# Optimization experiments

Hardware: AMD Instinct MI355X
Metric: run time of the kernel (lower is better)

Reference implementation:

```python
import jax, jax.numpy as jnp
import numpy as np

HEADS = 8
DIM_HEAD = 64
QLEVEL = 127.0  # symmetric int8: clamp to [-128, 127]


def fake_quant(x):
    """Symmetric per-tensor int8 fake quantization with straight-through estimator."""
    delta = jnp.max(jnp.abs(x)) / QLEVEL
    xq = jnp.clip(jnp.round(x / delta), -128.0, 127.0) * delta
    return x + jax.lax.stop_gradient(xq - x)


def setup_inputs() -> dict:
    key = jax.random.key(0)
    ks = jax.random.split(key, 7)
    b, n, m, d, dc = 2, 4096, 1024, 512, 768
    return {
        "x": jax.random.normal(ks[0], (b, n, d), jnp.float32),
        "context": jax.random.normal(ks[1], (b, m, dc), jnp.float32),
        "Wq": jax.random.normal(ks[2], (d, d), jnp.float32) * 0.02,
        "Wk": jax.random.normal(ks[3], (dc, d), jnp.float32) * 0.02,
        "Wv": jax.random.normal(ks[4], (dc, d), jnp.float32) * 0.02,
        "Wo": jax.random.normal(ks[5], (d, d), jnp.float32) * 0.02,
        "bo": jnp.zeros((d,), jnp.float32),
    }


def reference(x, context, Wq, Wk, Wv, Wo, bo):
    b, n, _ = x.shape
    h, dh = HEADS, DIM_HEAD
    scale = dh ** -0.5

    q = x @ Wq            # [b, n, h*dh]
    k = context @ Wk      # [b, m, h*dh]
    v = context @ Wv      # [b, m, h*dh]

    def split(t):  # b n (h d) -> b h n d
        return t.reshape(t.shape[0], t.shape[1], h, dh).transpose(0, 2, 1, 3)

    q, k, v = split(q), split(k), split(v)

    # fake-quantize q and k before the score matmul (use_aq=True path)
    q = fake_quant(q)
    k = fake_quant(k)
    sim = jnp.einsum('bhid,bhjd->bhij', q, k) * scale  # [b, h, n, m]
    attn = jax.nn.softmax(sim, axis=-1)

    # fake-quantize attention weights and v before the AV matmul
    out = jnp.einsum('bhij,bhjd->bhid', fake_quant(attn), fake_quant(v))
    out = out.transpose(0, 2, 1, 3).reshape(b, n, h * dh)  # b h n d -> b n (h d)
    return out @ Wo + bo  # to_out[0]; to_out[-1] is Dropout (identity in eval)
```

## Files before the change

### kernel.cpp

```cpp
#include <hip/hip_runtime.h>
#include <stdint.h>

typedef float  v4f  __attribute__((ext_vector_type(4)));
typedef int    v4i  __attribute__((ext_vector_type(4)));
typedef __bf16 v8bf __attribute__((ext_vector_type(8)));
typedef __bf16 v4bf __attribute__((ext_vector_type(4)));

#define BATCH  2
#define NQ     4096
#define MK     1024
#define DMODEL 512
#define DCTX   768
#define NH     8
#define DH     64

__global__ __launch_bounds__(256) void k_wtrans(
    const float* __restrict__ Wq, const float* __restrict__ Wk,
    const float* __restrict__ Wv, const float* __restrict__ Wo,
    __bf16* __restrict__ Wq_t, __bf16* __restrict__ Wk_t,
    __bf16* __restrict__ Wv_t, __bf16* __restrict__ Wo_t,
    unsigned* __restrict__ scal) {
  if (blockIdx.x == 0 && blockIdx.y == 0 && blockIdx.z == 0 && threadIdx.x < 4)
    scal[threadIdx.x] = 0u;
  const float* src; __bf16* dst; int K;
  switch (blockIdx.z) {
    case 0:  src = Wq; dst = Wq_t; K = DMODEL; break;
    case 1:  src = Wk; dst = Wk_t; K = DCTX;   break;
    case 2:  src = Wv; dst = Wv_t; K = DCTX;   break;
    default: src = Wo; dst = Wo_t; K = DMODEL; break;
  }
  int k0 = blockIdx.y * 32;
  if (k0 >= K) return;
  int n0 = blockIdx.x * 32;
  __shared__ __bf16 tile[32][33];
  int c = threadIdx.x & 31, r0 = threadIdx.x >> 5;
  for (int i = 0; i < 4; ++i) {
    int r = r0 + i * 8;
    tile[c][r] = (__bf16)src[(size_t)(k0 + r) * DMODEL + n0 + c];
  }
  __syncthreads();
  for (int i = 0; i < 4; ++i) {
    int r = r0 + i * 8;
    dst[(size_t)(n0 + r) * K + k0 + c] = tile[r][c];
  }
}

__global__ __launch_bounds__(256) void k_cvt(
    const float* __restrict__ x, const float* __restrict__ ctx,
    __bf16* __restrict__ xb, __bf16* __restrict__ cb) {
  const int XC = BATCH * NQ * DMODEL / 8;
  const int CC = BATCH * MK * DCTX / 8;
  int idx = blockIdx.x * 256 + threadIdx.x;
  const float* src; __bf16* dst;
  if (idx < XC) { src = x + (size_t)idx * 8; dst = xb + (size_t)idx * 8; }
  else {
    int j = idx - XC;
    if (j >= CC) return;
    src = ctx + (size_t)j * 8; dst = cb + (size_t)j * 8;
  }
  float4 a = *(const float4*)src, b = *(const float4*)(src + 4);
  v8bf o = { (__bf16)a.x, (__bf16)a.y, (__bf16)a.z, (__bf16)a.w,
             (__bf16)b.x, (__bf16)b.y, (__bf16)b.z, (__bf16)b.w };
  *(v8bf*)dst = o;
}

template<int K_, bool BIAS, bool AMAX>
__global__ __launch_bounds__(256, 3) void k_gemm_bs(
    const __bf16* __restrict__ A, const __bf16* __restrict__ Bt,
    float* __restrict__ C, int M, int N,
    const float* __restrict__ bias,
    unsigned* __restrict__ amaxLo, unsigned* __restrict__ amaxHi) {
  constexpr int CS = K_ + 8;
  constexpr int GPC = K_ / 8;
  __shared__ __bf16 Bs[32 * CS];
  __shared__ float redmax[4];
  const int tid = threadIdx.x;
  const int lane = tid & 63, wave = tid >> 6;
  const int l15 = lane & 15, g = lane >> 4;
  const int col0 = blockIdx.y * 32;
  const int row0w = blockIdx.x * 128 + wave * 32;

#pragma unroll
  for (int i = 0; i < GPC * 32 / 256; ++i) {
    int f = i * 256 + tid;
    int c = f / GPC, w = f - c * GPC;
    *(v8bf*)(&Bs[c * CS + w * 8]) =
        *(const v8bf*)(Bt + (size_t)(col0 + c) * K_ + w * 8);
  }
  __syncthreads();

  v4f acc[2][2] = {};
  const __bf16* a0 = A + (size_t)(row0w + l15) * K_ + g * 8;
  const __bf16* a1 = A + (size_t)(row0w + 16 + l15) * K_ + g * 8;
#pragma unroll
  for (int k0 = 0; k0 < K_; k0 += 32) {
    v8bf af0 = *(const v8bf*)(a0 + k0);
    v8bf af1 = *(const v8bf*)(a1 + k0);
    v8bf bf0 = *(const v8bf*)(&Bs[l15 * CS + k0 + g * 8]);
    v8bf bf1 = *(const v8bf*)(&Bs[(16 + l15) * CS + k0 + g * 8]);
    acc[0][0] = __builtin_amdgcn_mfma_f32_16x16x32_bf16(af0, bf0, acc[0][0], 0, 0, 0);
    acc[0][1] = __builtin_amdgcn_mfma_f32_16x16x32_bf16(af0, bf1, acc[0][1], 0, 0, 0);
    acc[1][0] = __builtin_amdgcn_mfma_f32_16x16x32_bf16(af1, bf0, acc[1][0], 0, 0, 0);
    acc[1][1] = __builtin_amdgcn_mfma_f32_16x16x32_bf16(af1, bf1, acc[1][1], 0, 0, 0);
  }

  float lmax = 0.0f;
#pragma unroll
  for (int j = 0; j < 2; ++j) {
    int col = col0 + j * 16 + l15;
    float bv = BIAS ? bias[col] : 0.0f;
#pragma unroll
    for (int i = 0; i < 2; ++i) {
#pragma unroll
      for (int r = 0; r < 4; ++r) {
        int row = row0w + i * 16 + g * 4 + r;
        float cv = acc[i][j][r] + bv;
        C[(size_t)row * N + col] = cv;
        if (AMAX) lmax = fmaxf(lmax, fabsf(cv));
      }
    }
  }
  if (AMAX) {
    for (int off = 32; off > 0; off >>= 1)
      lmax = fmaxf(lmax, __shfl_xor(lmax, off, 64));
    if (lane == 0) redmax[wave] = lmax;
    __syncthreads();
    if (tid == 0) {
      float bm = fmaxf(fmaxf(redmax[0], redmax[1]), fmaxf(redmax[2], redmax[3]));
      atomicMax(col0 < 512 ? amaxLo : amaxHi, __float_as_uint(bm));
    }
  }
}

__global__ __launch_bounds__(256) void k_quant_kv(
    const float* __restrict__ kvf,
    int8_t* __restrict__ k8, int8_t* __restrict__ v8t,
    const unsigned* __restrict__ scal) {
  __shared__ int8_t tile[64][80];
  int bx = blockIdx.x;
  if (bx < 1024) {
    int j = bx * 256 + threadIdx.x;
    int r = j >> 7;
    int c4 = (j & 127) << 2;
    float4 v = *(const float4*)(kvf + (size_t)r * 1024 + c4);
    float s = 127.0f / __uint_as_float(scal[1]);
    int a0 = __float2int_rn(v.x * s), a1 = __float2int_rn(v.y * s);
    int a2 = __float2int_rn(v.z * s), a3 = __float2int_rn(v.w * s);
    a0 = max(-128, min(127, a0)); a1 = max(-128, min(127, a1));
    a2 = max(-128, min(127, a2)); a3 = max(-128, min(127, a3));
    unsigned p = (unsigned)(a0 & 255) | ((unsigned)(a1 & 255) << 8) |
                 ((unsigned)(a2 & 255) << 16) | ((unsigned)(a3 & 255) << 24);
    *(unsigned*)(k8 + (size_t)j * 4) = p;
    return;
  }
  int id = bx - 1024;
  int bh = id >> 4, b = bh >> 3, h = bh & 7;
  int j0 = (id & 15) * 64;
  const float s = 127.0f / __uint_as_float(scal[2]);
  int t = threadIdx.x;
  int j = t >> 2, dh0 = (t & 3) << 4;
  const float* src = kvf + (size_t)(b * MK + j0 + j) * 1024 + 512 + h * DH + dh0;
#pragma unroll
  for (int i = 0; i < 16; i += 4) {
    float4 v = *(const float4*)(src + i);
    int a0 = __float2int_rn(v.x * s), a1 = __float2int_rn(v.y * s);
    int a2 = __float2int_rn(v.z * s), a3 = __float2int_rn(v.w * s);
    tile[dh0 + i + 0][j] = (int8_t)max(-128, min(127, a0));
    tile[dh0 + i + 1][j] = (int8_t)max(-128, min(127, a1));
    tile[dh0 + i + 2][j] = (int8_t)max(-128, min(127, a2));
    tile[dh0 + i + 3][j] = (int8_t)max(-128, min(127, a3));
  }
  __syncthreads();
  int dh = t >> 2, jb = (t & 3) << 4;
  v4i val = *(const v4i*)(&tile[dh][jb]);
  *(v4i*)(v8t + (size_t)(bh * DH + dh) * MK + j0 + jb) = val;
}

__device__ __forceinline__ v4i quant_pack16(const float* p, float s) {
  v4i out;
#pragma unroll
  for (int q = 0; q < 4; ++q) {
    float4 v = *(const float4*)(p + q * 4);
    int a0 = __float2int_rn(v.x * s), a1 = __float2int_rn(v.y * s);
    int a2 = __float2int_rn(v.z * s), a3 = __float2int_rn(v.w * s);
    a0 = max(-128, min(127, a0)); a1 = max(-128, min(127, a1));
    a2 = max(-128, min(127, a2)); a3 = max(-128, min(127, a3));
    out[q] = (int)((unsigned)(a0 & 255) | ((unsigned)(a1 & 255) << 8) |
                   ((unsigned)(a2 & 255) << 16) | ((unsigned)(a3 & 255) << 24));
  }
  return out;
}

__global__ __launch_bounds__(256, 4) void k_pass1(
    const float* __restrict__ qf, int8_t* __restrict__ q8,
    const int8_t* __restrict__ k8,
    float* __restrict__ invz, unsigned* __restrict__ scal) {
  __shared__ float zbuf[4][64];
  __shared__ int   mbuf[4][64];
  int bh = blockIdx.y, b = bh >> 3, h = bh & 7;
  int wave = threadIdx.x >> 6, lane = threadIdx.x & 63;
  int l15 = lane & 15, g = lane >> 4;
  int row0 = blockIdx.x * 64;
  const float aq = __uint_as_float(scal[0]), ak = __uint_as_float(scal[1]);
  const float alpha2 = (aq * ak) * (0.125f / (127.0f * 127.0f)) * 1.44269504f;
  const float sq = 127.0f / aq;
  const v4i z4 = {0, 0, 0, 0};
  v4i qfrag[4];
#pragma unroll
  for (int rg = 0; rg < 4; ++rg) {
    size_t off = (size_t)(b * NQ + row0 + rg * 16 + l15) * DMODEL + h * DH + g * 16;
    qfrag[rg] = quant_pack16(qf + off, sq);
    *(v4i*)(q8 + off) = qfrag[rg];
  }
  const int8_t* kbase = k8 + (size_t)b * MK * DMODEL + h * DH + g * 16 +
                        (size_t)wave * 256 * DMODEL;
  v4i kf[16];
#pragma unroll
  for (int i = 0; i < 16; ++i)
    kf[i] = *(const v4i*)(kbase + (size_t)(i * 16 + l15) * DMODEL);

  float z[4] = {0.f, 0.f, 0.f, 0.f};
  int mi[4] = {-(1 << 30), -(1 << 30), -(1 << 30), -(1 << 30)};
#pragma unroll
  for (int kt = 0; kt < 16; ++kt) {
#pragma unroll
    for (int rg = 0; rg < 4; ++rg) {
      v4i sa = __builtin_amdgcn_mfma_i32_16x16x64_i8(kf[kt], qfrag[rg], z4, 0, 0, 0);
      mi[rg] = max(mi[rg], max(max(sa[0], sa[1]), max(sa[2], sa[3])));
      float e0 = __builtin_amdgcn_exp2f((float)sa[0] * alpha2);
      float e1 = __builtin_amdgcn_exp2f((float)sa[1] * alpha2);
      float e2 = __builtin_amdgcn_exp2f((float)sa[2] * alpha2);
      float e3 = __builtin_amdgcn_exp2f((float)sa[3] * alpha2);
      z[rg] += (e0 + e1) + (e2 + e3);
    }
  }
#pragma unroll
  for (int rg = 0; rg < 4; ++rg) {
    z[rg] += __shfl_xor(z[rg], 16, 64);
    mi[rg] = max(mi[rg], __shfl_xor(mi[rg], 16, 64));
    z[rg] += __shfl_xor(z[rg], 32, 64);
    mi[rg] = max(mi[rg], __shfl_xor(mi[rg], 32, 64));
  }
  if (lane < 16) {
#pragma unroll
    for (int rg = 0; rg < 4; ++rg) {
      zbuf[wave][rg * 16 + l15] = z[rg];
      mbuf[wave][rg * 16 + l15] = mi[rg];
    }
  }
  __syncthreads();
  if (threadIdx.x < 64) {
    int r = threadIdx.x;
    float zt = (zbuf[0][r] + zbuf[1][r]) + (zbuf[2][r] + zbuf[3][r]);
    int mt = max(max(mbuf[0][r], mbuf[1][r]), max(mbuf[2][r], mbuf[3][r]));
    float iz = 1.0f / zt;
    invz[(size_t)bh * NQ + row0 + r] = iz;
    float ma = __builtin_amdgcn_exp2f((float)mt * alpha2) * iz;
    for (int off = 1; off < 64; off <<= 1)
      ma = fmaxf(ma, __shfl_xor(ma, off, 64));
    if (r == 0) atomicMax(scal + 3, __float_as_uint(ma));
  }
}

__global__ __launch_bounds__(256, 2) void k_pass2(
    const int8_t* __restrict__ q8, const int8_t* __restrict__ k8,
    const int8_t* __restrict__ v8t, const float* __restrict__ invz,
    const unsigned* __restrict__ scal, __bf16* __restrict__ o) {
  __shared__ __align__(16) int8_t attn_lds[4][16 * 80];
  __shared__ __align__(16) int redbuf[16][64][4];
  int bh = blockIdx.y, b = bh >> 3, h = bh & 7;
  int wave = threadIdx.x >> 6, lane = threadIdx.x & 63;
  int l15 = lane & 15, g = lane >> 4;
  int row0 = blockIdx.x * 64;
  int key0 = wave * 256;
  const float aq = __uint_as_float(scal[0]), ak = __uint_as_float(scal[1]);
  const float avv = __uint_as_float(scal[2]), izm = __uint_as_float(scal[3]);
  const float alpha2 = (aq * ak) * (0.125f / (127.0f * 127.0f)) * 1.44269504f;
  const float oscale = (izm / 127.0f) * (avv / 127.0f);
  const float MAGIC = 12582912.0f;
  const v4i z4 = {0, 0, 0, 0};

  v4i qfrag[4];
  float lc[4];
#pragma unroll
  for (int rg = 0; rg < 4; ++rg) {
    qfrag[rg] = *(const v4i*)(q8 + (size_t)(b * NQ + row0 + rg * 16 + l15) * DMODEL + h * DH + g * 16);
    lc[rg] = __builtin_amdgcn_logf(invz[(size_t)bh * NQ + row0 + rg * 16 + l15] * (127.0f / izm));
  }
  const int8_t* kbase = k8 + (size_t)(b * MK + key0) * DMODEL + h * DH + g * 16;
  v4i kf[16];
#pragma unroll
  for (int i = 0; i < 16; ++i)
    kf[i] = *(const v4i*)(kbase + (size_t)(i * 16 + l15) * DMODEL);
  const int8_t* vbase = v8t + (size_t)bh * DH * MK + key0 + g * 16;
  v4i vf[16];
#pragma unroll
  for (int d = 0; d < 4; ++d)
#pragma unroll
    for (int c = 0; c < 4; ++c)
      vf[d * 4 + c] = *(const v4i*)(vbase + (size_t)(d * 16 + l15) * MK + c * 64);

  int8_t* alds = attn_lds[wave];
  __bf16* obase = o + (size_t)(b * NQ + row0) * DMODEL + h * DH;

#pragma unroll
  for (int rg = 0; rg < 4; ++rg) {
    const float lcr = lc[rg];
    v4i pacc[4] = {};
#pragma unroll
    for (int c = 0; c < 4; ++c) {
#pragma unroll
      for (int t = 0; t < 4; ++t) {
        v4i sa = __builtin_amdgcn_mfma_i32_16x16x64_i8(kf[c * 4 + t], qfrag[rg], z4, 0, 0, 0);
        float f0 = __builtin_amdgcn_exp2f(fmaf((float)sa[0], alpha2, lcr)) + MAGIC;
        float f1 = __builtin_amdgcn_exp2f(fmaf((float)sa[1], alpha2, lcr)) + MAGIC;
        float f2 = __builtin_amdgcn_exp2f(fmaf((float)sa[2], alpha2, lcr)) + MAGIC;
        float f3 = __builtin_amdgcn_exp2f(fmaf((float)sa[3], alpha2, lcr)) + MAGIC;
        unsigned packed = (__float_as_uint(f0) & 255u) |
                          ((__float_as_uint(f1) & 255u) << 8) |
                          ((__float_as_uint(f2) & 255u) << 16) |
                          (__float_as_uint(f3) << 24);
        *(unsigned*)(alds + l15 * 80 + t * 16 + g * 4) = packed;
      }
      v4i afrag = *(const v4i*)(alds + l15 * 80 + g * 16);
#pragma unroll
      for (int d = 0; d < 4; ++d)
        pacc[d] = __builtin_amdgcn_mfma_i32_16x16x64_i8(afrag, vf[d * 4 + c], pacc[d], 0, 0, 0);
    }
    __syncthreads();
#pragma unroll
    for (int d = 0; d < 4; ++d)
      *(v4i*)(&redbuf[wave * 4 + d][lane][0]) = pacc[d];
    __syncthreads();
    v4i s0 = *(const v4i*)(&redbuf[wave][lane][0]);
    v4i s1 = *(const v4i*)(&redbuf[4 + wave][lane][0]);
    v4i s2 = *(const v4i*)(&redbuf[8 + wave][lane][0]);
    v4i s3 = *(const v4i*)(&redbuf[12 + wave][lane][0]);
    v4i sum = (s0 + s1) + (s2 + s3);
#pragma unroll
    for (int r = 0; r < 4; ++r) {
      int row = rg * 16 + (lane >> 4) * 4 + r;
      obase[(size_t)row * DMODEL + wave * 16 + (lane & 15)] =
          (__bf16)((float)sum[r] * oscale);
    }
  }
}

extern "C" void kernel_launch(void* const* d_in, const int* in_sizes, int n_in,
                              void* d_out, int out_size, void* d_ws, size_t ws_size,
                              hipStream_t stream) {
  (void)in_sizes; (void)n_in; (void)out_size; (void)ws_size;
  const float* x   = (const float*)d_in[0];
  const float* ctx = (const float*)d_in[1];
  const float* Wq  = (const float*)d_in[2];
  const float* Wk  = (const float*)d_in[3];
  const float* Wv  = (const float*)d_in[4];
  const float* Wo  = (const float*)d_in[5];
  const float* bo  = (const float*)d_in[6];
  float* out = (float*)d_out;

  char* ws = (char*)d_ws;
  size_t off = 0;
  auto alloc = [&](size_t bytes) {
    char* p = ws + off;
    off += (bytes + 255) & ~(size_t)255;
    return p;
  };
  unsigned* scal = (unsigned*)alloc(16);
  __bf16* Wq_t = (__bf16*)alloc((size_t)512 * 512 * 2);
  __bf16* Wk_t = (__bf16*)alloc((size_t)512 * 768 * 2);
  __bf16* Wv_t = (__bf16*)alloc((size_t)512 * 768 * 2);
  __bf16* Wo_t = (__bf16*)alloc((size_t)512 * 512 * 2);
  __bf16* xb   = (__bf16*)alloc((size_t)BATCH * NQ * DMODEL * 2);
  __bf16* cb   = (__bf16*)alloc((size_t)BATCH * MK * DCTX * 2);
  float* qf  = (float*)alloc((size_t)BATCH * NQ * DMODEL * 4);
  float* kvf = (float*)alloc((size_t)BATCH * MK * 1024 * 4);
  int8_t* q8 = (int8_t*)alloc((size_t)BATCH * NQ * DMODEL);
  int8_t* k8 = (int8_t*)alloc((size_t)BATCH * MK * DMODEL);
  int8_t* v8t = (int8_t*)alloc((size_t)BATCH * NH * DH * MK);
  float* invz = (float*)alloc((size_t)BATCH * NH * NQ * 4);
  __bf16* o = (__bf16*)qf;

  k_wtrans<<<dim3(16, 24, 4), 256, 0, stream>>>(Wq, Wk, Wv, Wo, Wq_t, Wk_t, Wv_t, Wo_t, scal);
  k_cvt<<<2816, 256, 0, stream>>>(x, ctx, xb, cb);
  k_gemm_bs<512, false, true><<<dim3(64, 16), 256, 0, stream>>>(
      xb, Wq_t, qf, 8192, 512, nullptr, scal + 0, scal + 0);
  k_gemm_bs<768, false, true><<<dim3(16, 32), 256, 0, stream>>>(
      cb, Wk_t, kvf, 2048, 1024, nullptr, scal + 1, scal + 2);
  k_quant_kv<<<1280, 256, 0, stream>>>(kvf, k8, v8t, scal);
  k_pass1<<<dim3(64, 16), 256, 0, stream>>>(qf, q8, k8, invz, scal);
  k_pass2<<<dim3(64, 16), 256, 0, stream>>>(q8, k8, v8t, invz, scal, o);
  k_gemm_bs<512, true, false><<<dim3(64, 16), 256, 0, stream>>>(
      o, Wo_t, out, 8192, 512, bo, nullptr, nullptr);
}
```

Before: 204.3 us.

## Repartition attention passes so each wave owns query rows and stream K/V tiles via LDS

Both the softmax-normalizer pass and the attention pass now give each wave 16 query rows over all keys, instead of splitting keys across waves. K (and, in pass2, transposed V) are staged cooperatively through LDS tiles of 128 keys. This removes the cross-wave LDS reduction of partial outputs and the large per-thread K/V register arrays, and raises pass2 occupancy from 2 to 4 blocks per SIMD. In exchange it adds per-tile barriers and LDS fragment reads, and the exp/quantize work is no longer spread over keys within a block.

Measured after the change: 201.8 us. No clear change (-1.2%).

```diff
diff --git a/kernel.cpp b/kernel.cpp
--- a/kernel.cpp
+++ b/kernel.cpp
@@ -195,84 +195,80 @@
     const float* __restrict__ qf, int8_t* __restrict__ q8,
     const int8_t* __restrict__ k8,
     float* __restrict__ invz, unsigned* __restrict__ scal) {
-  __shared__ float zbuf[4][64];
-  __shared__ int   mbuf[4][64];
+  __shared__ __align__(16) int8_t kbuf[128 * 72];
+  __shared__ float mared[4];
   int bh = blockIdx.y, b = bh >> 3, h = bh & 7;
   int wave = threadIdx.x >> 6, lane = threadIdx.x & 63;
   int l15 = lane & 15, g = lane >> 4;
   int row0 = blockIdx.x * 64;
+  int myrow = row0 + wave * 16 + l15;
   const float aq = __uint_as_float(scal[0]), ak = __uint_as_float(scal[1]);
   const float alpha2 = (aq * ak) * (0.125f / (127.0f * 127.0f)) * 1.44269504f;
   const float sq = 127.0f / aq;
   const v4i z4 = {0, 0, 0, 0};
-  v4i qfrag[4];
-#pragma unroll
-  for (int rg = 0; rg < 4; ++rg) {
-    size_t off = (size_t)(b * NQ + row0 + rg * 16 + l15) * DMODEL + h * DH + g * 16;
-    qfrag[rg] = quant_pack16(qf + off, sq);
-    *(v4i*)(q8 + off) = qfrag[rg];
-  }
-  const int8_t* kbase = k8 + (size_t)b * MK * DMODEL + h * DH + g * 16 +
-                        (size_t)wave * 256 * DMODEL;
-  v4i kf[16];
-#pragma unroll
-  for (int i = 0; i < 16; ++i)
-    kf[i] = *(const v4i*)(kbase + (size_t)(i * 16 + l15) * DMODEL);
+  size_t qoff = (size_t)(b * NQ + myrow) * DMODEL + h * DH + g * 16;
+  v4i qfrag = quant_pack16(qf + qoff, sq);
+  *(v4i*)(q8 + qoff) = qfrag;
+  const int8_t* kbase = k8 + (size_t)b * MK * DMODEL + h * DH;
+  const int rs = threadIdx.x >> 2, qs = (threadIdx.x & 3) * 16;
 
   float z[4] = {0.f, 0.f, 0.f, 0.f};
-  int mi[4] = {-(1 << 30), -(1 << 30), -(1 << 30), -(1 << 30)};
-#pragma unroll
-  for (int kt = 0; kt < 16; ++kt) {
-#pragma unroll
-    for (int rg = 0; rg < 4; ++rg) {
-      v4i sa = __builtin_amdgcn_mfma_i32_16x16x64_i8(kf[kt], qfrag[rg], z4, 0, 0, 0);
-      mi[rg] = max(mi[rg], max(max(sa[0], sa[1]), max(sa[2], sa[3])));
+  int mi = -(1 << 30);
+  for (int tile = 0; tile < 8; ++tile) {
+    __syncthreads();
+    *(v4i*)(&kbuf[rs * 72 + qs]) =
+        *(const v4i*)(kbase + (size_t)(tile * 128 + rs) * DMODEL + qs);
+    *(v4i*)(&kbuf[(rs + 64) * 72 + qs]) =
+        *(const v4i*)(kbase + (size_t)(tile * 128 + rs + 64) * DMODEL + qs);
+    __syncthreads();
+    float zt = z[tile >> 1];
+#pragma unroll
+    for (int t = 0; t < 8; ++t) {
+      v4i kfrag = *(const v4i*)(&kbuf[(t * 16 + l15) * 72 + g * 16]);
+      v4i sa = __builtin_amdgcn_mfma_i32_16x16x64_i8(kfrag, qfrag, z4, 0, 0, 0);
+      mi = max(mi, max(max(sa[0], sa[1]), max(sa[2], sa[3])));
       float e0 = __builtin_amdgcn_exp2f((float)sa[0] * alpha2);
       float e1 = __builtin_amdgcn_exp2f((float)sa[1] * alpha2);
       float e2 = __builtin_amdgcn_exp2f((float)sa[2] * alpha2);
       float e3 = __builtin_amdgcn_exp2f((float)sa[3] * alpha2);
-      z[rg] += (e0 + e1) + (e2 + e3);
-    }
-  }
-#pragma unroll
-  for (int rg = 0; rg < 4; ++rg) {
-    z[rg] += __shfl_xor(z[rg], 16, 64);
-    mi[rg] = max(mi[rg], __shfl_xor(mi[rg], 16, 64));
-    z[rg] += __shfl_xor(z[rg], 32, 64);
-    mi[rg] = max(mi[rg], __shfl_xor(mi[rg], 32, 64));
-  }
-  if (lane < 16) {
-#pragma unroll
-    for (int rg = 0; rg < 4; ++rg) {
-      zbuf[wave][rg * 16 + l15] = z[rg];
-      mbuf[wave][rg * 16 + l15] = mi[rg];
-    }
-  }
+      zt += (e0 + e1) + (e2 + e3);
+    }
+    z[tile >> 1] = zt;
+  }
+#pragma unroll
+  for (int i = 0; i < 4; ++i) {
+    z[i] += __shfl_xor(z[i], 16, 64);
+    z[i] += __shfl_xor(z[i], 32, 64);
+  }
+  mi = max(mi, __shfl_xor(mi, 16, 64));
+  mi = max(mi, __shfl_xor(mi, 32, 64));
+  float zt = (z[0] + z[1]) + (z[2] + z[3]);
+  float iz = 1.0f / zt;
+  if (g == 0) invz[(size_t)bh * NQ + myrow] = iz;
+  float ma = __builtin_amdgcn_exp2f((float)mi * alpha2) * iz;
+#pragma unroll
+  for (int off = 1; off < 16; off <<= 1)
+    ma = fmaxf(ma, __shfl_xor(ma, off, 64));
+  if (lane == 0) mared[wave] = ma;
   __syncthreads();
-  if (threadIdx.x < 64) {
-    int r = threadIdx.x;
-    float zt = (zbuf[0][r] + zbuf[1][r]) + (zbuf[2][r] + zbuf[3][r]);
-    int mt = max(max(mbuf[0][r], mbuf[1][r]), max(mbuf[2][r], mbuf[3][r]));
-    float iz = 1.0f / zt;
-    invz[(size_t)bh * NQ + row0 + r] = iz;
-    float ma = __builtin_amdgcn_exp2f((float)mt * alpha2) * iz;
-    for (int off = 1; off < 64; off <<= 1)
-      ma = fmaxf(ma, __shfl_xor(ma, off, 64));
-    if (r == 0) atomicMax(scal + 3, __float_as_uint(ma));
-  }
-}
-
-__global__ __launch_bounds__(256, 2) void k_pass2(
+  if (threadIdx.x == 0)
+    atomicMax(scal + 3,
+              __float_as_uint(fmaxf(fmaxf(mared[0], mared[1]),
+                                    fmaxf(mared[2], mared[3]))));
+}
+
+__global__ __launch_bounds__(256, 4) void k_pass2(
     const int8_t* __restrict__ q8, const int8_t* __restrict__ k8,
     const int8_t* __restrict__ v8t, const float* __restrict__ invz,
     const unsigned* __restrict__ scal, __bf16* __restrict__ o) {
-  __shared__ __align__(16) int8_t attn_lds[4][16 * 80];
-  __shared__ __align__(16) int redbuf[16][64][4];
+  __shared__ __align__(16) int8_t kbuf[128 * 72];
+  __shared__ __align__(16) int8_t vbuf[64 * 152];
+  __shared__ __align__(16) int8_t albuf[4][16 * 152];
   int bh = blockIdx.y, b = bh >> 3, h = bh & 7;
   int wave = threadIdx.x >> 6, lane = threadIdx.x & 63;
   int l15 = lane & 15, g = lane >> 4;
   int row0 = blockIdx.x * 64;
-  int key0 = wave * 256;
+  int myrow = row0 + wave * 16 + l15;
   const float aq = __uint_as_float(scal[0]), ak = __uint_as_float(scal[1]);
   const float avv = __uint_as_float(scal[2]), izm = __uint_as_float(scal[3]);
   const float alpha2 = (aq * ak) * (0.125f / (127.0f * 127.0f)) * 1.44269504f;
@@ -280,70 +276,57 @@
   const float MAGIC = 12582912.0f;
   const v4i z4 = {0, 0, 0, 0};
 
-  v4i qfrag[4];
-  float lc[4];
-#pragma unroll
-  for (int rg = 0; rg < 4; ++rg) {
-    qfrag[rg] = *(const v4i*)(q8 + (size_t)(b * NQ + row0 + rg * 16 + l15) * DMODEL + h * DH + g * 16);
-    lc[rg] = __builtin_amdgcn_logf(invz[(size_t)bh * NQ + row0 + rg * 16 + l15] * (127.0f / izm));
-  }
-  const int8_t* kbase = k8 + (size_t)(b * MK + key0) * DMODEL + h * DH + g * 16;
-  v4i kf[16];
-#pragma unroll
-  for (int i = 0; i < 16; ++i)
-    kf[i] = *(const v4i*)(kbase + (size_t)(i * 16 + l15) * DMODEL);
-  const int8_t* vbase = v8t + (size_t)bh * DH * MK + key0 + g * 16;
-  v4i vf[16];
+  v4i qfrag = *(const v4i*)(q8 + (size_t)(b * NQ + myrow) * DMODEL + h * DH + g * 16);
+  const float lcr = __builtin_amdgcn_logf(invz[(size_t)bh * NQ + myrow] * (127.0f / izm));
+  const int8_t* kbase = k8 + (size_t)b * MK * DMODEL + h * DH;
+  const int8_t* vbase = v8t + (size_t)bh * DH * MK;
+  int8_t* alds = albuf[wave];
+  const int rs = threadIdx.x >> 2, qs = (threadIdx.x & 3) * 16;
+  const int vr = threadIdx.x >> 3, vq = (threadIdx.x & 7) * 16;
+
+  v4i pacc[4] = {};
+  for (int tile = 0; tile < 8; ++tile) {
+    __syncthreads();
+    *(v4i*)(&kbuf[rs * 72 + qs]) =
+        *(const v4i*)(kbase + (size_t)(tile * 128 + rs) * DMODEL + qs);
+    *(v4i*)(&kbuf[(rs + 64) * 72 + qs]) =
+        *(const v4i*)(kbase + (size_t)(tile * 128 + rs + 64) * DMODEL + qs);
+    *(v4i*)(&vbuf[vr * 152 + vq]) =
+        *(const v4i*)(vbase + (size_t)vr * MK + tile * 128 + vq);
+    *(v4i*)(&vbuf[(vr + 32) * 152 + vq]) =
+        *(const v4i*)(vbase + (size_t)(vr + 32) * MK + tile * 128 + vq);
+    __syncthreads();
+#pragma unroll
+    for (int t = 0; t < 8; ++t) {
+      v4i kfrag = *(const v4i*)(&kbuf[(t * 16 + l15) * 72 + g * 16]);
+      v4i sa = __builtin_amdgcn_mfma_i32_16x16x64_i8(kfrag, qfrag, z4, 0, 0, 0);
+      float f0 = __builtin_amdgcn_exp2f(fmaf((float)sa[0], alpha2, lcr)) + MAGIC;
+      float f1 = __builtin_amdgcn_exp2f(fmaf((float)sa[1], alpha2, lcr)) + MAGIC;
+      float f2 = __builtin_amdgcn_exp2f(fmaf((float)sa[2], alpha2, lcr)) + MAGIC;
+      float f3 = __builtin_amdgcn_exp2f(fmaf((float)sa[3], alpha2, lcr)) + MAGIC;
+      unsigned packed = (__float_as_uint(f0) & 255u) |
+                        ((__float_as_uint(f1) & 255u) << 8) |
+                        ((__float_as_uint(f2) & 255u) << 16) |
+                        (__float_as_uint(f3) << 24);
+      *(unsigned*)(alds + l15 * 152 + t * 16 + g * 4) = packed;
+    }
+#pragma unroll
+    for (int c = 0; c < 2; ++c) {
+      v4i afrag = *(const v4i*)(alds + l15 * 152 + c * 64 + g * 16);
+#pragma unroll
+      for (int d = 0; d < 4; ++d) {
+        v4i bfrag = *(const v4i*)(&vbuf[(d * 16 + l15) * 152 + c * 64 + g * 16]);
+        pacc[d] = __builtin_amdgcn_mfma_i32_16x16x64_i8(afrag, bfrag, pacc[d], 0, 0, 0);
+      }
+    }
+  }
+  __bf16* obase = o + (size_t)(b * NQ + row0 + wave * 16) * DMODEL + h * DH;
 #pragma unroll
   for (int d = 0; d < 4; ++d)
 #pragma unroll
-    for (int c = 0; c < 4; ++c)
-      vf[d * 4 + c] = *(const v4i*)(vbase + (size_t)(d * 16 + l15) * MK + c * 64);
-
-  int8_t* alds = attn_lds[wave];
-  __bf16* obase = o + (size_t)(b * NQ + row0) * DMODEL + h * DH;
-
-#pragma unroll
-  for (int rg = 0; rg < 4; ++rg) {
-    const float lcr = lc[rg];
-    v4i pacc[4] = {};
-#pragma unroll
-    for (int c = 0; c < 4; ++c) {
-#pragma unroll
-      for (int t = 0; t < 4; ++t) {
-        v4i sa = __builtin_amdgcn_mfma_i32_16x16x64_i8(kf[c * 4 + t], qfrag[rg], z4, 0, 0, 0);
-        float f0 = __builtin_amdgcn_exp2f(fmaf((float)sa[0], alpha2, lcr)) + MAGIC;
-        float f1 = __builtin_amdgcn_exp2f(fmaf((float)sa[1], alpha2, lcr)) + MAGIC;
-        float f2 = __builtin_amdgcn_exp2f(fmaf((float)sa[2], alpha2, lcr)) + MAGIC;
-        float f3 = __builtin_amdgcn_exp2f(fmaf((float)sa[3], alpha2, lcr)) + MAGIC;
-        unsigned packed = (__float_as_uint(f0) & 255u) |
-                          ((__float_as_uint(f1) & 255u) << 8) |
-                          ((__float_as_uint(f2) & 255u) << 16) |
-                          (__float_as_uint(f3) << 24);
-        *(unsigned*)(alds + l15 * 80 + t * 16 + g * 4) = packed;
-      }
-      v4i afrag = *(const v4i*)(alds + l15 * 80 + g * 16);
-#pragma unroll
-      for (int d = 0; d < 4; ++d)
-        pacc[d] = __builtin_amdgcn_mfma_i32_16x16x64_i8(afrag, vf[d * 4 + c], pacc[d], 0, 0, 0);
-    }
-    __syncthreads();
-#pragma unroll
-    for (int d = 0; d < 4; ++d)
-      *(v4i*)(&redbuf[wave * 4 + d][lane][0]) = pacc[d];
-    __syncthreads();
-    v4i s0 = *(const v4i*)(&redbuf[wave][lane][0]);
-    v4i s1 = *(const v4i*)(&redbuf[4 + wave][lane][0]);
-    v4i s2 = *(const v4i*)(&redbuf[8 + wave][lane][0]);
-    v4i s3 = *(const v4i*)(&redbuf[12 + wave][lane][0]);
-    v4i sum = (s0 + s1) + (s2 + s3);
-#pragma unroll
-    for (int r = 0; r < 4; ++r) {
-      int row = rg * 16 + (lane >> 4) * 4 + r;
-      obase[(size_t)row * DMODEL + wave * 16 + (lane & 15)] =
-          (__bf16)((float)sum[r] * oscale);
-    }
-  }
+    for (int r = 0; r < 4; ++r)
+      obase[(size_t)(g * 4 + r) * DMODEL + d * 16 + l15] =
+          (__bf16)((float)pacc[d][r] * oscale);
 }
 
 extern "C" void kernel_launch(void* const* d_in, const int* in_sizes, int n_in,
```
